# Kernel optimization log

Hardware: AMD Instinct MI355X
Metric: run time of the kernel (lower is better)

Reference implementation:

```python
import jax, jax.numpy as jnp
import numpy as np
import math

NUM_HEADS = 16
THETA = 10000.0


def _rope(x):
    # x: (B, L, H, hd); interleaved-pair rotary embedding
    B, L, H, hd = x.shape
    inv_freq = 1.0 / (THETA ** (jnp.arange(0, hd, 2, dtype=jnp.float32) / hd))  # (hd/2,)
    ang = jnp.arange(L, dtype=jnp.float32)[:, None] * inv_freq[None, :]         # (L, hd/2)
    cos = jnp.cos(ang)[None, :, None, :].astype(x.dtype)
    sin = jnp.sin(ang)[None, :, None, :].astype(x.dtype)
    x1 = x[..., 0::2]
    x2 = x[..., 1::2]
    r1 = x1 * cos - x2 * sin
    r2 = x1 * sin + x2 * cos
    return jnp.stack([r1, r2], axis=-1).reshape(x.shape)


def setup_inputs() -> dict:
    key = jax.random.key(0)
    ks = jax.random.split(key, 5)
    B, L, D = 4, 2048, 1024
    x = jax.random.normal(ks[0], (B, L, D), dtype=jnp.float32)
    scale = 0.02
    wq = jax.random.normal(ks[1], (D, D), dtype=jnp.float32) * scale
    wk = jax.random.normal(ks[2], (D, D), dtype=jnp.float32) * scale
    wv = jax.random.normal(ks[3], (D, D), dtype=jnp.float32) * scale
    wo = jax.random.normal(ks[4], (D, D), dtype=jnp.float32) * scale
    return {"x": x, "wq": wq, "wk": wk, "wv": wv, "wo": wo}


def reference(x, wq, wk, wv, wo):
    B, L, D = x.shape
    H = NUM_HEADS
    hd = D // H
    q = (x @ wq).reshape(B, L, H, hd)
    k = (x @ wk).reshape(B, L, H, hd)
    v = (x @ wv).reshape(B, L, H, hd)
    q = _rope(q)
    k = _rope(k)
    # (B, H, L, hd)
    q = q.transpose(0, 2, 1, 3)
    k = k.transpose(0, 2, 1, 3)
    v = v.transpose(0, 2, 1, 3)
    # default-mask path of forward(): float 0/1 mask over key positions added to scores
    mask = (jnp.sum(x, axis=-1) != 0).astype(x.dtype)[:, None, None, :]  # (B,1,1,L)
    scale_factor = 1.0 / math.sqrt(hd)
    scores = jnp.einsum("bhld,bhsd->bhls", q, k) * scale_factor + mask
    attn = jax.nn.softmax(scores, axis=-1)
    out = jnp.einsum("bhls,bhsd->bhld", attn, v)          # (B,H,L,hd)
    out = out.transpose(0, 2, 1, 3).reshape(B, L, D)
    return out @ wo
```

## Files before the change

kernel.cpp:

```cpp
#include <hip/hip_runtime.h>

typedef __bf16 bf16_t;
typedef bf16_t bf16x8 __attribute__((ext_vector_type(8)));
typedef bf16_t bf16x4 __attribute__((ext_vector_type(4)));
typedef bf16_t bf16x2 __attribute__((ext_vector_type(2)));
typedef float f32x4 __attribute__((ext_vector_type(4)));
typedef float f32x16 __attribute__((ext_vector_type(16)));
typedef unsigned int uint32x4 __attribute__((ext_vector_type(4)));

__device__ __forceinline__ ushort f2bu(float f) {
  unsigned u = __float_as_uint(f);
  unsigned r = (u + 0x7fffu + ((u >> 16) & 1u)) >> 16;
  return (ushort)r;
}
__device__ __forceinline__ float b2f(ushort u) {
  return __uint_as_float(((unsigned)u) << 16);
}

typedef const __attribute__((address_space(1))) unsigned int* gas_ptr;
typedef __attribute__((address_space(3))) unsigned int* las_ptr;
__device__ __forceinline__ void g2l16(const void* g, void* l) {
  __builtin_amdgcn_global_load_lds((gas_ptr)g, (las_ptr)l, 16, 0, 0);
}

__global__ __launch_bounds__(256) void pack_x(const float* __restrict__ x,
                                              ushort* __restrict__ xb,
                                              float* __restrict__ maskv) {
  int row = blockIdx.x;
  int tid = threadIdx.x;
  const float4 v = ((const float4*)(x + (size_t)row * 1024))[tid];
  ushort4 o;
  o.x = f2bu(v.x); o.y = f2bu(v.y); o.z = f2bu(v.z); o.w = f2bu(v.w);
  ((ushort4*)(xb + (size_t)row * 1024))[tid] = o;
  float s = v.x + v.y + v.z + v.w;
#pragma unroll
  for (int m = 1; m < 64; m <<= 1) s += __shfl_xor(s, m);
  __shared__ float wsum[4];
  if ((tid & 63) == 0) wsum[tid >> 6] = s;
  __syncthreads();
  if (tid == 0)
    maskv[row] = ((wsum[0] + wsum[1] + wsum[2] + wsum[3]) != 0.f)
                     ? 1.4426950408889634f : 0.f;
}

__global__ __launch_bounds__(1024) void pack_w(const float* __restrict__ w,
                                               ushort* __restrict__ wt) {
  __shared__ float t[32][33];
  int n0 = blockIdx.x * 32, k0 = blockIdx.y * 32;
  int tx = threadIdx.x, ty = threadIdx.y;
  t[ty][tx] = w[(size_t)(k0 + ty) * 1024 + n0 + tx];
  __syncthreads();
  wt[(size_t)(n0 + ty) * 1024 + k0 + tx] = f2bu(t[tx][ty]);
}

__global__ __launch_bounds__(256) void gemm_bf16(const ushort* __restrict__ A,
                                                 const ushort* __restrict__ BT,
                                                 void* __restrict__ Cv,
                                                 int M, int N, int K, int mode) {
  __shared__ ushort lA[128 * 64];
  __shared__ ushort lB[128 * 64];
  const int tid = threadIdx.x;
  const int wave = tid >> 6, lane = tid & 63;
  const int lr = lane & 15, lk = lane >> 4;
  const int bm = blockIdx.x * 128, bn = blockIdx.y * 128;
  const int wr = (wave >> 1) * 64, wc = (wave & 1) * 64;
  f32x4 acc[4][4] = {};
  for (int kt = 0; kt < K; kt += 64) {
#pragma unroll
    for (int t = 0; t < 4; ++t) {
      int e = (t * 256 + tid) * 8;
      int row = e >> 6, col = e & 63;
      g2l16(A + (size_t)(bm + row) * K + kt + col, lA + e);
      g2l16(BT + (size_t)(bn + row) * K + kt + col, lB + e);
    }
    __syncthreads();
#pragma unroll
    for (int ks = 0; ks < 2; ++ks) {
      bf16x8 af[4], bfr[4];
#pragma unroll
      for (int i = 0; i < 4; ++i)
        af[i] = *(const bf16x8*)(lA + (wr + i * 16 + lr) * 64 + ks * 32 + lk * 8);
#pragma unroll
      for (int j = 0; j < 4; ++j)
        bfr[j] = *(const bf16x8*)(lB + (wc + j * 16 + lr) * 64 + ks * 32 + lk * 8);
#pragma unroll
      for (int i = 0; i < 4; ++i)
#pragma unroll
        for (int j = 0; j < 4; ++j)
          acc[i][j] = __builtin_amdgcn_mfma_f32_16x16x32_bf16(af[i], bfr[j],
                                                              acc[i][j], 0, 0, 0);
    }
    __syncthreads();
  }
#pragma unroll
  for (int i = 0; i < 4; ++i)
#pragma unroll
    for (int j = 0; j < 4; ++j)
#pragma unroll
      for (int r = 0; r < 4; ++r) {
        int m = bm + wr + i * 16 + lk * 4 + r;
        int n = bn + wc + j * 16 + lr;
        float v = acc[i][j][r];
        if (mode == 2) {
          ((float*)Cv)[(size_t)m * N + n] = v;
        } else {
          int b = m >> 11, l = m & 2047;
          int h = n >> 6, d = n & 63;
          size_t addr;
          if (mode == 0) addr = (((size_t)b * 16 + h) * 2048 + l) * 64 + d;
          else           addr = (((size_t)b * 16 + h) * 64 + d) * 2048 + l;
          ((ushort*)Cv)[addr] = f2bu(v);
        }
      }
}

__global__ __launch_bounds__(256) void rope_k(ushort* __restrict__ Qb,
                                              ushort* __restrict__ Kb) {
  const size_t P1 = (size_t)64 * 2048 * 32;
  size_t id = (size_t)blockIdx.x * 256 + threadIdx.x;
  ushort* base = Qb;
  size_t rr = id;
  if (id >= P1) { base = Kb; rr = id - P1; }
  int i = (int)(rr & 31);
  int l = (int)((rr >> 5) & 2047);
  size_t bh = rr >> 16;
  size_t addr = (bh * 2048 + (size_t)l) * 64 + 2 * i;
  unsigned p = *(const unsigned*)(base + addr);
  float x1 = b2f((ushort)(p & 0xffffu));
  float x2 = b2f((ushort)(p >> 16));
  const float c = 0.41524101186092029f;
  float inv = exp2f(-c * (float)i);
  float ang = (float)l * inv;
  float sv, cv;
  sincosf(ang, &sv, &cv);
  float r1 = x1 * cv - x2 * sv;
  float r2 = x1 * sv + x2 * cv;
  unsigned o = (unsigned)f2bu(r1) | ((unsigned)f2bu(r2) << 16);
  *(unsigned*)(base + addr) = o;
}

__global__ __launch_bounds__(512, 4) void attn_k(const ushort* __restrict__ Qb,
                                                 const ushort* __restrict__ Kb,
                                                 const ushort* __restrict__ VTb,
                                                 const float* __restrict__ maskv,
                                                 ushort* __restrict__ Ob) {
  __shared__ ushort lK[2][4096];
  __shared__ ushort lV[2][4096];
  const int tid = threadIdx.x;
  const int wid = tid >> 6, lane = tid & 63;
  const int q = lane & 31, hi = lane >> 5;
  int f = blockIdx.x;
  int swz = (f & 7) * 64 + (f >> 3);
  int qb_i = swz & 7, bh = swz >> 3;
  int b = bh >> 4, h = bh & 15;
  const int q0w = qb_i * 256 + wid * 32;
  const ushort* qp = Qb + (size_t)bh * 2048 * 64;
  const ushort* kp = Kb + (size_t)bh * 2048 * 64;
  const ushort* vp = VTb + (size_t)bh * 64 * 2048;
  const float SCL = 0.18033688011112042f;

  bf16x8 qfr[4];
#pragma unroll
  for (int s = 0; s < 4; ++s)
    qfr[s] = *(const bf16x8*)(qp + (size_t)(q0w + q) * 64 + s * 16 + hi * 8);

  f32x16 oacc[2] = {};
  float m2 = -1e30f, ls = 0.f;

  const int sr = tid >> 3;
  const int ss = (tid & 7) ^ (sr & 7);
  const ushort* kg = kp + sr * 64 + ss * 8;
  const ushort* vg = vp + (size_t)sr * 2048 + ss * 8;
  int roff[4];
#pragma unroll
  for (int j = 0; j < 4; ++j)
    roff[j] = q * 128 + (((2 * j + hi) ^ (q & 7)) << 4);

  g2l16(kg, (char*)lK + tid * 16);
  g2l16(vg, (char*)lV + tid * 16);
  __syncthreads();

  int cur = 0;
  for (int kt = 0; kt < 32; ++kt) {
    if (kt < 31) {
      g2l16(kg + (kt + 1) * 4096, (char*)lK + (cur ^ 1) * 8192 + tid * 16);
      g2l16(vg + (kt + 1) * 64,   (char*)lV + (cur ^ 1) * 8192 + tid * 16);
    }
    const char* bK = (const char*)lK + cur * 8192;
    f32x16 sacc[2] = {};
#pragma unroll
    for (int kb2 = 0; kb2 < 2; ++kb2)
#pragma unroll
      for (int s = 0; s < 4; ++s) {
        bf16x8 kfr = *(const bf16x8*)(bK + kb2 * 4096 + roff[s]);
        sacc[kb2] = __builtin_amdgcn_mfma_f32_32x32x16_bf16(kfr, qfr[s],
                                                            sacc[kb2], 0, 0, 0);
      }
    const float* mbase = maskv + (size_t)b * 2048 + kt * 64;
#pragma unroll
    for (int kb2 = 0; kb2 < 2; ++kb2)
#pragma unroll
      for (int g = 0; g < 4; ++g) {
        f32x4 mv = *(const f32x4*)(mbase + kb2 * 32 + g * 8 + 4 * hi);
#pragma unroll
        for (int e = 0; e < 4; ++e)
          sacc[kb2][4 * g + e] = sacc[kb2][4 * g + e] * SCL + mv[e];
      }
    float mx = -1e30f;
#pragma unroll
    for (int r = 0; r < 16; ++r) mx = fmaxf(mx, fmaxf(sacc[0][r], sacc[1][r]));
    mx = fmaxf(mx, __shfl_xor(mx, 32));
    float mnew = fmaxf(m2, mx);
    float corr = __builtin_amdgcn_exp2f(m2 - mnew);
    m2 = mnew;
    float ps = 0.f;
#pragma unroll
    for (int kb2 = 0; kb2 < 2; ++kb2)
#pragma unroll
      for (int r = 0; r < 16; ++r) {
        float p = __builtin_amdgcn_exp2f(sacc[kb2][r] - mnew);
        sacc[kb2][r] = p;
        ps += p;
      }
    ps += __shfl_xor(ps, 32);
    ls = ls * corr + ps;
#pragma unroll
    for (int d2 = 0; d2 < 2; ++d2)
#pragma unroll
      for (int r = 0; r < 16; ++r) oacc[d2][r] *= corr;

    const char* bV = (const char*)lV + cur * 8192;
#pragma unroll
    for (int kb2 = 0; kb2 < 2; ++kb2) {
      unsigned w[8];
#pragma unroll
      for (int j = 0; j < 8; ++j) {
        bf16x2 t2;
        t2[0] = (bf16_t)sacc[kb2][2 * j];
        t2[1] = (bf16_t)sacc[kb2][2 * j + 1];
        w[j] = __builtin_bit_cast(unsigned, t2);
      }
#pragma unroll
      for (int sg = 0; sg < 2; ++sg) {
        unsigned X0 = (unsigned)__shfl_xor((int)w[4 * sg + 0], 32);
        unsigned X1 = (unsigned)__shfl_xor((int)w[4 * sg + 1], 32);
        unsigned X2 = (unsigned)__shfl_xor((int)w[4 * sg + 2], 32);
        unsigned X3 = (unsigned)__shfl_xor((int)w[4 * sg + 3], 32);
        uint32x4 fw;
        fw[0] = hi ? X2 : w[4 * sg + 0];
        fw[1] = hi ? X3 : w[4 * sg + 1];
        fw[2] = hi ? w[4 * sg + 2] : X0;
        fw[3] = hi ? w[4 * sg + 3] : X1;
        bf16x8 pfr = __builtin_bit_cast(bf16x8, fw);
        int tau = kb2 * 2 + sg;
#pragma unroll
        for (int d2 = 0; d2 < 2; ++d2) {
          bf16x8 vfr = *(const bf16x8*)(bV + d2 * 4096 + roff[tau]);
          oacc[d2] = __builtin_amdgcn_mfma_f32_32x32x16_bf16(vfr, pfr,
                                                             oacc[d2], 0, 0, 0);
        }
      }
    }
    __syncthreads();
    cur ^= 1;
  }

  float inv = 1.f / ls;
  const int l = q0w + q;
#pragma unroll
  for (int d2 = 0; d2 < 2; ++d2)
#pragma unroll
    for (int g = 0; g < 4; ++g) {
      ushort4 o;
      o.x = f2bu(oacc[d2][4 * g + 0] * inv);
      o.y = f2bu(oacc[d2][4 * g + 1] * inv);
      o.z = f2bu(oacc[d2][4 * g + 2] * inv);
      o.w = f2bu(oacc[d2][4 * g + 3] * inv);
      int dcol = d2 * 32 + g * 8 + 4 * hi;
      *(ushort4*)(Ob + ((size_t)b * 2048 + l) * 1024 + h * 64 + dcol) = o;
    }
}

extern "C" void kernel_launch(void* const* d_in, const int* in_sizes, int n_in,
                              void* d_out, int out_size, void* d_ws, size_t ws_size,
                              hipStream_t stream) {
  const float* x  = (const float*)d_in[0];
  const float* wq = (const float*)d_in[1];
  const float* wk = (const float*)d_in[2];
  const float* wv = (const float*)d_in[3];
  const float* wo = (const float*)d_in[4];
  float* out = (float*)d_out;
  char* ws = (char*)d_ws;
  const size_t MB = 1024 * 1024;
  ushort* xb   = (ushort*)(ws);
  ushort* ao   = (ushort*)(ws);
  ushort* wqT  = (ushort*)(ws + 16 * MB);
  ushort* wkT  = (ushort*)(ws + 18 * MB);
  ushort* wvT  = (ushort*)(ws + 20 * MB);
  ushort* woT  = (ushort*)(ws + 22 * MB);
  ushort* qb   = (ushort*)(ws + 24 * MB);
  ushort* kb   = (ushort*)(ws + 40 * MB);
  ushort* vtb  = (ushort*)(ws + 56 * MB);
  float* maskv = (float*)(ws + 72 * MB);

  pack_x<<<8192, 256, 0, stream>>>(x, xb, maskv);
  dim3 tb(32, 32);
  pack_w<<<dim3(32, 32), tb, 0, stream>>>(wq, wqT);
  pack_w<<<dim3(32, 32), tb, 0, stream>>>(wk, wkT);
  pack_w<<<dim3(32, 32), tb, 0, stream>>>(wv, wvT);
  pack_w<<<dim3(32, 32), tb, 0, stream>>>(wo, woT);
  gemm_bf16<<<dim3(64, 8), 256, 0, stream>>>(xb, wqT, qb, 8192, 1024, 1024, 0);
  gemm_bf16<<<dim3(64, 8), 256, 0, stream>>>(xb, wkT, kb, 8192, 1024, 1024, 0);
  gemm_bf16<<<dim3(64, 8), 256, 0, stream>>>(xb, wvT, vtb, 8192, 1024, 1024, 1);
  rope_k<<<32768, 256, 0, stream>>>(qb, kb);
  attn_k<<<512, 512, 0, stream>>>(qb, kb, vtb, maskv, ao);
  gemm_bf16<<<dim3(64, 8), 256, 0, stream>>>(ao, woT, out, 8192, 1024, 1024, 2);
}
```

Baseline: 353.7 us.

## Fuse QKV GEMMs with RoPE epilogue and add lazy softmax rescale

Result: slower. 809.0 us (+128.7%).

```diff
diff --git a/kernel.cpp b/kernel.cpp
--- a/kernel.cpp
+++ b/kernel.cpp
@@ -53,25 +53,28 @@
   wt[(size_t)(n0 + ty) * 1024 + k0 + tx] = f2bu(t[tx][ty]);
 }
 
-__global__ __launch_bounds__(256) void gemm_bf16(const ushort* __restrict__ A,
-                                                 const ushort* __restrict__ BT,
-                                                 void* __restrict__ Cv,
-                                                 int M, int N, int K, int mode) {
+__global__ __launch_bounds__(256) void qkv_gemm(const ushort* __restrict__ A,
+                                                const ushort* __restrict__ BT,
+                                                ushort* __restrict__ Qo,
+                                                ushort* __restrict__ Ko,
+                                                ushort* __restrict__ VTo) {
   __shared__ ushort lA[128 * 64];
   __shared__ ushort lB[128 * 64];
   const int tid = threadIdx.x;
   const int wave = tid >> 6, lane = tid & 63;
   const int lr = lane & 15, lk = lane >> 4;
-  const int bm = blockIdx.x * 128, bn = blockIdx.y * 128;
+  const int f = blockIdx.x;
+  const int wgid = (f & 7) * 192 + (f >> 3);
+  const int bm = (wgid & 63) * 128, bn = (wgid >> 6) * 128;
   const int wr = (wave >> 1) * 64, wc = (wave & 1) * 64;
   f32x4 acc[4][4] = {};
-  for (int kt = 0; kt < K; kt += 64) {
+  for (int kt = 0; kt < 1024; kt += 64) {
 #pragma unroll
     for (int t = 0; t < 4; ++t) {
       int e = (t * 256 + tid) * 8;
       int row = e >> 6, col = e & 63;
-      g2l16(A + (size_t)(bm + row) * K + kt + col, lA + e);
-      g2l16(BT + (size_t)(bn + row) * K + kt + col, lB + e);
+      g2l16(A + (size_t)(bm + row) * 1024 + kt + col, lA + e);
+      g2l16(BT + (size_t)(bn + row) * 1024 + kt + col, lB + e);
     }
     __syncthreads();
 #pragma unroll
@@ -92,6 +95,94 @@
     }
     __syncthreads();
   }
+  const int which = bn >> 10;
+  const float SCL = 0.18033688011112042f;
+  const float cc = 0.41524101186092029f;
+  if (which < 2) {
+    ushort* dst = which ? Ko : Qo;
+    float invf[4];
+#pragma unroll
+    for (int j = 0; j < 4; ++j) {
+      int d = (wc + j * 16 + lr) & 63;
+      invf[j] = exp2f(-cc * (float)(d >> 1));
+    }
+#pragma unroll
+    for (int i = 0; i < 4; ++i)
+#pragma unroll
+      for (int r = 0; r < 4; ++r) {
+        int m = bm + wr + i * 16 + lk * 4 + r;
+        int b = m >> 11, l = m & 2047;
+#pragma unroll
+        for (int j = 0; j < 4; ++j) {
+          int c10 = (bn + wc + j * 16 + lr) & 1023;
+          int h = c10 >> 6, d = c10 & 63;
+          float v = acc[i][j][r];
+          float pv = __shfl_xor(v, 1);
+          float sv, cv;
+          sincosf((float)l * invf[j], &sv, &cv);
+          float out = (d & 1) ? (pv * sv + v * cv)
+                              : (v * cv - pv * sv);
+          if (which == 0) out *= SCL;
+          dst[(((size_t)b * 16 + h) * 2048 + l) * 64 + d] = f2bu(out);
+        }
+      }
+  } else {
+#pragma unroll
+    for (int i = 0; i < 4; ++i)
+#pragma unroll
+      for (int r = 0; r < 4; ++r) {
+        int m = bm + wr + i * 16 + lk * 4 + r;
+        int b = m >> 11, l = m & 2047;
+#pragma unroll
+        for (int j = 0; j < 4; ++j) {
+          int c10 = (bn + wc + j * 16 + lr) & 1023;
+          int h = c10 >> 6, d = c10 & 63;
+          VTo[(((size_t)b * 16 + h) * 64 + d) * 2048 + l] = f2bu(acc[i][j][r]);
+        }
+      }
+  }
+}
+
+__global__ __launch_bounds__(256) void wo_gemm(const ushort* __restrict__ A,
+                                               const ushort* __restrict__ BT,
+                                               float* __restrict__ C) {
+  __shared__ ushort lA[128 * 64];
+  __shared__ ushort lB[128 * 64];
+  const int tid = threadIdx.x;
+  const int wave = tid >> 6, lane = tid & 63;
+  const int lr = lane & 15, lk = lane >> 4;
+  const int f = blockIdx.x;
+  const int wgid = (f & 7) * 64 + (f >> 3);
+  const int bm = (wgid & 63) * 128, bn = (wgid >> 6) * 128;
+  const int wr = (wave >> 1) * 64, wc = (wave & 1) * 64;
+  f32x4 acc[4][4] = {};
+  for (int kt = 0; kt < 1024; kt += 64) {
+#pragma unroll
+    for (int t = 0; t < 4; ++t) {
+      int e = (t * 256 + tid) * 8;
+      int row = e >> 6, col = e & 63;
+      g2l16(A + (size_t)(bm + row) * 1024 + kt + col, lA + e);
+      g2l16(BT + (size_t)(bn + row) * 1024 + kt + col, lB + e);
+    }
+    __syncthreads();
+#pragma unroll
+    for (int ks = 0; ks < 2; ++ks) {
+      bf16x8 af[4], bfr[4];
+#pragma unroll
+      for (int i = 0; i < 4; ++i)
+        af[i] = *(const bf16x8*)(lA + (wr + i * 16 + lr) * 64 + ks * 32 + lk * 8);
+#pragma unroll
+      for (int j = 0; j < 4; ++j)
+        bfr[j] = *(const bf16x8*)(lB + (wc + j * 16 + lr) * 64 + ks * 32 + lk * 8);
+#pragma unroll
+      for (int i = 0; i < 4; ++i)
+#pragma unroll
+        for (int j = 0; j < 4; ++j)
+          acc[i][j] = __builtin_amdgcn_mfma_f32_16x16x32_bf16(af[i], bfr[j],
+                                                              acc[i][j], 0, 0, 0);
+    }
+    __syncthreads();
+  }
 #pragma unroll
   for (int i = 0; i < 4; ++i)
 #pragma unroll
@@ -100,43 +191,8 @@
       for (int r = 0; r < 4; ++r) {
         int m = bm + wr + i * 16 + lk * 4 + r;
         int n = bn + wc + j * 16 + lr;
-        float v = acc[i][j][r];
-        if (mode == 2) {
-          ((float*)Cv)[(size_t)m * N + n] = v;
-        } else {
-          int b = m >> 11, l = m & 2047;
-          int h = n >> 6, d = n & 63;
-          size_t addr;
-          if (mode == 0) addr = (((size_t)b * 16 + h) * 2048 + l) * 64 + d;
-          else           addr = (((size_t)b * 16 + h) * 64 + d) * 2048 + l;
-          ((ushort*)Cv)[addr] = f2bu(v);
-        }
-      }
-}
-
-__global__ __launch_bounds__(256) void rope_k(ushort* __restrict__ Qb,
-                                              ushort* __restrict__ Kb) {
-  const size_t P1 = (size_t)64 * 2048 * 32;
-  size_t id = (size_t)blockIdx.x * 256 + threadIdx.x;
-  ushort* base = Qb;
-  size_t rr = id;
-  if (id >= P1) { base = Kb; rr = id - P1; }
-  int i = (int)(rr & 31);
-  int l = (int)((rr >> 5) & 2047);
-  size_t bh = rr >> 16;
-  size_t addr = (bh * 2048 + (size_t)l) * 64 + 2 * i;
-  unsigned p = *(const unsigned*)(base + addr);
-  float x1 = b2f((ushort)(p & 0xffffu));
-  float x2 = b2f((ushort)(p >> 16));
-  const float c = 0.41524101186092029f;
-  float inv = exp2f(-c * (float)i);
-  float ang = (float)l * inv;
-  float sv, cv;
-  sincosf(ang, &sv, &cv);
-  float r1 = x1 * cv - x2 * sv;
-  float r2 = x1 * sv + x2 * cv;
-  unsigned o = (unsigned)f2bu(r1) | ((unsigned)f2bu(r2) << 16);
-  *(unsigned*)(base + addr) = o;
+        C[(size_t)m * 1024 + n] = acc[i][j][r];
+      }
 }
 
 __global__ __launch_bounds__(512, 4) void attn_k(const ushort* __restrict__ Qb,
@@ -157,7 +213,6 @@
   const ushort* qp = Qb + (size_t)bh * 2048 * 64;
   const ushort* kp = Kb + (size_t)bh * 2048 * 64;
   const ushort* vp = VTb + (size_t)bh * 64 * 2048;
-  const float SCL = 0.18033688011112042f;
 
   bf16x8 qfr[4];
 #pragma unroll
@@ -188,6 +243,7 @@
     }
     const char* bK = (const char*)lK + cur * 8192;
     f32x16 sacc[2] = {};
+    __builtin_amdgcn_s_setprio(1);
 #pragma unroll
     for (int kb2 = 0; kb2 < 2; ++kb2)
 #pragma unroll
@@ -196,6 +252,7 @@
         sacc[kb2] = __builtin_amdgcn_mfma_f32_32x32x16_bf16(kfr, qfr[s],
                                                             sacc[kb2], 0, 0, 0);
       }
+    __builtin_amdgcn_s_setprio(0);
     const float* mbase = maskv + (size_t)b * 2048 + kt * 64;
 #pragma unroll
     for (int kb2 = 0; kb2 < 2; ++kb2)
@@ -203,33 +260,41 @@
       for (int g = 0; g < 4; ++g) {
         f32x4 mv = *(const f32x4*)(mbase + kb2 * 32 + g * 8 + 4 * hi);
 #pragma unroll
-        for (int e = 0; e < 4; ++e)
-          sacc[kb2][4 * g + e] = sacc[kb2][4 * g + e] * SCL + mv[e];
+        for (int e = 0; e < 4; ++e) sacc[kb2][4 * g + e] += mv[e];
       }
     float mx = -1e30f;
 #pragma unroll
     for (int r = 0; r < 16; ++r) mx = fmaxf(mx, fmaxf(sacc[0][r], sacc[1][r]));
     mx = fmaxf(mx, __shfl_xor(mx, 32));
-    float mnew = fmaxf(m2, mx);
-    float corr = __builtin_amdgcn_exp2f(m2 - mnew);
-    m2 = mnew;
+    const bool skip = __all(mx - m2 <= 8.f);
+    float corr = 1.f;
+    if (!skip) {
+      float mnew = fmaxf(m2, mx);
+      corr = __builtin_amdgcn_exp2f(m2 - mnew);
+      m2 = mnew;
+    }
     float ps = 0.f;
 #pragma unroll
     for (int kb2 = 0; kb2 < 2; ++kb2)
 #pragma unroll
       for (int r = 0; r < 16; ++r) {
-        float p = __builtin_amdgcn_exp2f(sacc[kb2][r] - mnew);
+        float p = __builtin_amdgcn_exp2f(sacc[kb2][r] - m2);
         sacc[kb2][r] = p;
         ps += p;
       }
     ps += __shfl_xor(ps, 32);
-    ls = ls * corr + ps;
-#pragma unroll
-    for (int d2 = 0; d2 < 2; ++d2)
-#pragma unroll
-      for (int r = 0; r < 16; ++r) oacc[d2][r] *= corr;
+    if (skip) {
+      ls += ps;
+    } else {
+      ls = ls * corr + ps;
+#pragma unroll
+      for (int d2 = 0; d2 < 2; ++d2)
+#pragma unroll
+        for (int r = 0; r < 16; ++r) oacc[d2][r] *= corr;
+    }
 
     const char* bV = (const char*)lV + cur * 8192;
+    __builtin_amdgcn_s_setprio(1);
 #pragma unroll
     for (int kb2 = 0; kb2 < 2; ++kb2) {
       unsigned w[8];
@@ -242,15 +307,12 @@
       }
 #pragma unroll
       for (int sg = 0; sg < 2; ++sg) {
-        unsigned X0 = (unsigned)__shfl_xor((int)w[4 * sg + 0], 32);
-        unsigned X1 = (unsigned)__shfl_xor((int)w[4 * sg + 1], 32);
-        unsigned X2 = (unsigned)__shfl_xor((int)w[4 * sg + 2], 32);
-        unsigned X3 = (unsigned)__shfl_xor((int)w[4 * sg + 3], 32);
+        unsigned a0 = w[4 * sg + 0], b0 = w[4 * sg + 2];
+        unsigned a1 = w[4 * sg + 1], b1 = w[4 * sg + 3];
+        asm("v_permlane32_swap_b32 %0, %1" : "+v"(a0), "+v"(b0));
+        asm("v_permlane32_swap_b32 %0, %1" : "+v"(a1), "+v"(b1));
         uint32x4 fw;
-        fw[0] = hi ? X2 : w[4 * sg + 0];
-        fw[1] = hi ? X3 : w[4 * sg + 1];
-        fw[2] = hi ? w[4 * sg + 2] : X0;
-        fw[3] = hi ? w[4 * sg + 3] : X1;
+        fw[0] = a0; fw[1] = a1; fw[2] = b0; fw[3] = b1;
         bf16x8 pfr = __builtin_bit_cast(bf16x8, fw);
         int tau = kb2 * 2 + sg;
 #pragma unroll
@@ -261,6 +323,7 @@
         }
       }
     }
+    __builtin_amdgcn_s_setprio(0);
     __syncthreads();
     cur ^= 1;
   }
@@ -292,27 +355,22 @@
   float* out = (float*)d_out;
   char* ws = (char*)d_ws;
   const size_t MB = 1024 * 1024;
-  ushort* xb   = (ushort*)(ws);
-  ushort* ao   = (ushort*)(ws);
-  ushort* wqT  = (ushort*)(ws + 16 * MB);
-  ushort* wkT  = (ushort*)(ws + 18 * MB);
-  ushort* wvT  = (ushort*)(ws + 20 * MB);
-  ushort* woT  = (ushort*)(ws + 22 * MB);
-  ushort* qb   = (ushort*)(ws + 24 * MB);
-  ushort* kb   = (ushort*)(ws + 40 * MB);
-  ushort* vtb  = (ushort*)(ws + 56 * MB);
-  float* maskv = (float*)(ws + 72 * MB);
+  ushort* xb    = (ushort*)(ws);
+  ushort* ao    = (ushort*)(ws);
+  ushort* wqkvT = (ushort*)(ws + 16 * MB);
+  ushort* woT   = (ushort*)(ws + 22 * MB);
+  ushort* qb    = (ushort*)(ws + 24 * MB);
+  ushort* kb    = (ushort*)(ws + 40 * MB);
+  ushort* vtb   = (ushort*)(ws + 56 * MB);
+  float* maskv  = (float*)(ws + 72 * MB);
 
   pack_x<<<8192, 256, 0, stream>>>(x, xb, maskv);
   dim3 tb(32, 32);
-  pack_w<<<dim3(32, 32), tb, 0, stream>>>(wq, wqT);
-  pack_w<<<dim3(32, 32), tb, 0, stream>>>(wk, wkT);
-  pack_w<<<dim3(32, 32), tb, 0, stream>>>(wv, wvT);
+  pack_w<<<dim3(32, 32), tb, 0, stream>>>(wq, wqkvT);
+  pack_w<<<dim3(32, 32), tb, 0, stream>>>(wk, wqkvT + 1024 * 1024);
+  pack_w<<<dim3(32, 32), tb, 0, stream>>>(wv, wqkvT + 2048 * 1024);
   pack_w<<<dim3(32, 32), tb, 0, stream>>>(wo, woT);
-  gemm_bf16<<<dim3(64, 8), 256, 0, stream>>>(xb, wqT, qb, 8192, 1024, 1024, 0);
-  gemm_bf16<<<dim3(64, 8), 256, 0, stream>>>(xb, wkT, kb, 8192, 1024, 1024, 0);
-  gemm_bf16<<<dim3(64, 8), 256, 0, stream>>>(xb, wvT, vtb, 8192, 1024, 1024, 1);
-  rope_k<<<32768, 256, 0, stream>>>(qb, kb);
+  qkv_gemm<<<1536, 256, 0, stream>>>(xb, wqkvT, qb, kb, vtb);
   attn_k<<<512, 512, 0, stream>>>(qb, kb, vtb, maskv, ao);
-  gemm_bf16<<<dim3(64, 8), 256, 0, stream>>>(ao, woT, out, 8192, 1024, 1024, 2);
-}
+  wo_gemm<<<512, 256, 0, stream>>>(ao, woT, out);
+}
```

## Fold softmax scale into RoPE, lazy rescale, permlane swap, MFMA priority

Applied to the files above, without the earlier changes.

After: 342.0 us. 1.03x faster.

```diff
diff --git a/kernel.cpp b/kernel.cpp
--- a/kernel.cpp
+++ b/kernel.cpp
@@ -120,7 +120,8 @@
   size_t id = (size_t)blockIdx.x * 256 + threadIdx.x;
   ushort* base = Qb;
   size_t rr = id;
-  if (id >= P1) { base = Kb; rr = id - P1; }
+  bool isQ = true;
+  if (id >= P1) { base = Kb; rr = id - P1; isQ = false; }
   int i = (int)(rr & 31);
   int l = (int)((rr >> 5) & 2047);
   size_t bh = rr >> 16;
@@ -135,6 +136,10 @@
   sincosf(ang, &sv, &cv);
   float r1 = x1 * cv - x2 * sv;
   float r2 = x1 * sv + x2 * cv;
+  if (isQ) {
+    const float SCL = 0.18033688011112042f;
+    r1 *= SCL; r2 *= SCL;
+  }
   unsigned o = (unsigned)f2bu(r1) | ((unsigned)f2bu(r2) << 16);
   *(unsigned*)(base + addr) = o;
 }
@@ -157,7 +162,6 @@
   const ushort* qp = Qb + (size_t)bh * 2048 * 64;
   const ushort* kp = Kb + (size_t)bh * 2048 * 64;
   const ushort* vp = VTb + (size_t)bh * 64 * 2048;
-  const float SCL = 0.18033688011112042f;
 
   bf16x8 qfr[4];
 #pragma unroll
@@ -188,6 +192,7 @@
     }
     const char* bK = (const char*)lK + cur * 8192;
     f32x16 sacc[2] = {};
+    __builtin_amdgcn_s_setprio(1);
 #pragma unroll
     for (int kb2 = 0; kb2 < 2; ++kb2)
 #pragma unroll
@@ -196,6 +201,7 @@
         sacc[kb2] = __builtin_amdgcn_mfma_f32_32x32x16_bf16(kfr, qfr[s],
                                                             sacc[kb2], 0, 0, 0);
       }
+    __builtin_amdgcn_s_setprio(0);
     const float* mbase = maskv + (size_t)b * 2048 + kt * 64;
 #pragma unroll
     for (int kb2 = 0; kb2 < 2; ++kb2)
@@ -203,33 +209,41 @@
       for (int g = 0; g < 4; ++g) {
         f32x4 mv = *(const f32x4*)(mbase + kb2 * 32 + g * 8 + 4 * hi);
 #pragma unroll
-        for (int e = 0; e < 4; ++e)
-          sacc[kb2][4 * g + e] = sacc[kb2][4 * g + e] * SCL + mv[e];
+        for (int e = 0; e < 4; ++e) sacc[kb2][4 * g + e] += mv[e];
       }
     float mx = -1e30f;
 #pragma unroll
     for (int r = 0; r < 16; ++r) mx = fmaxf(mx, fmaxf(sacc[0][r], sacc[1][r]));
     mx = fmaxf(mx, __shfl_xor(mx, 32));
-    float mnew = fmaxf(m2, mx);
-    float corr = __builtin_amdgcn_exp2f(m2 - mnew);
-    m2 = mnew;
+    const bool skip = __all(mx - m2 <= 8.f);
+    float corr = 1.f;
+    if (!skip) {
+      float mnew = fmaxf(m2, mx);
+      corr = __builtin_amdgcn_exp2f(m2 - mnew);
+      m2 = mnew;
+    }
     float ps = 0.f;
 #pragma unroll
     for (int kb2 = 0; kb2 < 2; ++kb2)
 #pragma unroll
       for (int r = 0; r < 16; ++r) {
-        float p = __builtin_amdgcn_exp2f(sacc[kb2][r] - mnew);
+        float p = __builtin_amdgcn_exp2f(sacc[kb2][r] - m2);
         sacc[kb2][r] = p;
         ps += p;
       }
     ps += __shfl_xor(ps, 32);
-    ls = ls * corr + ps;
-#pragma unroll
-    for (int d2 = 0; d2 < 2; ++d2)
-#pragma unroll
-      for (int r = 0; r < 16; ++r) oacc[d2][r] *= corr;
+    if (skip) {
+      ls += ps;
+    } else {
+      ls = ls * corr + ps;
+#pragma unroll
+      for (int d2 = 0; d2 < 2; ++d2)
+#pragma unroll
+        for (int r = 0; r < 16; ++r) oacc[d2][r] *= corr;
+    }
 
     const char* bV = (const char*)lV + cur * 8192;
+    __builtin_amdgcn_s_setprio(1);
 #pragma unroll
     for (int kb2 = 0; kb2 < 2; ++kb2) {
       unsigned w[8];
@@ -242,15 +256,12 @@
       }
 #pragma unroll
       for (int sg = 0; sg < 2; ++sg) {
-        unsigned X0 = (unsigned)__shfl_xor((int)w[4 * sg + 0], 32);
-        unsigned X1 = (unsigned)__shfl_xor((int)w[4 * sg + 1], 32);
-        unsigned X2 = (unsigned)__shfl_xor((int)w[4 * sg + 2], 32);
-        unsigned X3 = (unsigned)__shfl_xor((int)w[4 * sg + 3], 32);
+        unsigned a0 = w[4 * sg + 0], b0 = w[4 * sg + 2];
+        unsigned a1 = w[4 * sg + 1], b1 = w[4 * sg + 3];
+        asm("v_permlane32_swap_b32 %0, %1" : "+v"(a0), "+v"(b0));
+        asm("v_permlane32_swap_b32 %0, %1" : "+v"(a1), "+v"(b1));
         uint32x4 fw;
-        fw[0] = hi ? X2 : w[4 * sg + 0];
-        fw[1] = hi ? X3 : w[4 * sg + 1];
-        fw[2] = hi ? w[4 * sg + 2] : X0;
-        fw[3] = hi ? w[4 * sg + 3] : X1;
+        fw[0] = a0; fw[1] = a1; fw[2] = b0; fw[3] = b1;
         bf16x8 pfr = __builtin_bit_cast(bf16x8, fw);
         int tau = kb2 * 2 + sg;
 #pragma unroll
@@ -261,6 +272,7 @@
         }
       }
     }
+    __builtin_amdgcn_s_setprio(0);
     __syncthreads();
     cur ^= 1;
   }
```
